# Optimization experiments

Measured on AMD Instinct MI355X. Metric: run time of the kernel, lower is better.

The kernel has to match this reference:

```python
import math
import jax, jax.numpy as jnp
import numpy as np

NUM_HEADS = 12
HEAD_DIM = 64
HIDDEN = NUM_HEADS * HEAD_DIM  # 768
SEQ = 4096


def setup_inputs() -> dict:
    key = jax.random.key(0)
    ks = jax.random.split(key, 7)
    s = 0.02  # BERT-style init scale for weights
    return {
        "hidden_states": jax.random.normal(ks[0], (1, SEQ, HIDDEN), jnp.float32),
        "Wq": jax.random.normal(ks[1], (HIDDEN, HIDDEN), jnp.float32) * s,
        "bq": jax.random.normal(ks[2], (HIDDEN,), jnp.float32) * s,
        "Wk": jax.random.normal(ks[3], (HIDDEN, HIDDEN), jnp.float32) * s,
        "bk": jax.random.normal(ks[4], (HIDDEN,), jnp.float32) * s,
        "Wv": jax.random.normal(ks[5], (HIDDEN, HIDDEN), jnp.float32) * s,
        "bv": jax.random.normal(ks[6], (HIDDEN,), jnp.float32) * s,
    }


def _split_heads(z):
    # [S, HIDDEN] -> [H, S, dh]
    S = z.shape[0]
    return jnp.transpose(z.reshape(S, NUM_HEADS, HEAD_DIM), (1, 0, 2))


def reference(hidden_states, Wq, bq, Wk, bk, Wv, bv):
    # batch is squeezed in the original module (kernel is unbatched)
    x = hidden_states[0]  # [S, D]
    q = _split_heads(x @ Wq.T + bq)  # [H, S, dh]
    k = _split_heads(x @ Wk.T + bk)  # [H, S, dh]
    scale = 1.0 / math.sqrt(HEAD_DIM)
    scores = jnp.einsum('hqd,hkd->hqk', q, k) * scale  # [H, S, S]
    probs = jax.nn.softmax(scores, axis=-1)
    # multi_rand_attn_cuda approximates P @ (x @ Wv^T + bv) via CDF-driven
    # Monte-Carlo column sampling of Wv; its expectation is the exact product,
    # which is the correctness baseline computed here.
    v = _split_heads(x @ Wv.T + bv)  # [H, S, dh]
    ctx = jnp.einsum('hqk,hkd->hqd', probs, v)  # [H, S, dh]
    ctx = jnp.transpose(ctx, (1, 0, 2)).reshape(x.shape[0], HIDDEN)
    return ctx[None]  # [1, S, D]
```

## Files before the change

### kernel.cpp

```cpp
#include <hip/hip_runtime.h>
#include <stdint.h>


typedef float    f32x4 __attribute__((ext_vector_type(4)));
typedef _Float16 h16x8 __attribute__((ext_vector_type(8)));
typedef unsigned short u16;

#define MFMA_F16(A, B, C) __builtin_amdgcn_mfma_f32_16x16x32_f16((A), (B), (C), 0, 0, 0)
#define ZERO4 ((f32x4){0.f, 0.f, 0.f, 0.f})

#define SEQ 4096
#define HID 768
#define NH  12
#define DH  64

__device__ __forceinline__ u16 f2h(float f) {
  union { _Float16 h; u16 u; } v;
  v.h = (_Float16)f;
  return v.u;
}
__device__ __forceinline__ float h2f(u16 u) {
  union { u16 u; _Float16 h; } v;
  v.u = u;
  return (float)v.h;
}

__device__ __forceinline__ void gload_lds16(const void* g, void* l) {
  __builtin_amdgcn_global_load_lds(
      (__attribute__((address_space(1))) void*)(g),
      (__attribute__((address_space(3))) void*)(l),
      16, 0, 0);
}

__global__ __launch_bounds__(256) void cast_all_k(
    const float* __restrict__ x,  const float* __restrict__ wq,
    const float* __restrict__ wk, const float* __restrict__ wv,
    u16* __restrict__ xh,  u16* __restrict__ wqh,
    u16* __restrict__ wkh, u16* __restrict__ wvh)
{
  int i = blockIdx.x * 256 + threadIdx.x;
  const int NX4 = (SEQ * HID) / 4;
  const int NW4 = (HID * HID) / 4;
  const float4* src; ushort4* dst; int idx;
  if (i < NX4) {
    src = (const float4*)x; dst = (ushort4*)xh; idx = i;
  } else {
    int j = i - NX4;
    int w = j / NW4;
    idx = j - w * NW4;
    src = (const float4*)(w == 0 ? wq : (w == 1 ? wk : wv));
    dst = (ushort4*)(w == 0 ? wqh : (w == 1 ? wkh : wvh));
  }
  float4 v = src[idx];
  ushort4 o;
  o.x = f2h(v.x); o.y = f2h(v.y); o.z = f2h(v.z); o.w = f2h(v.w);
  dst[idx] = o;
}

__global__ __launch_bounds__(256, 2) void qkv_gemm_k(
    const u16* __restrict__ xh,
    const u16* __restrict__ wqh, const u16* __restrict__ wkh, const u16* __restrict__ wvh,
    const float* __restrict__ bq, const float* __restrict__ bk, const float* __restrict__ bv,
    u16* __restrict__ Qh, u16* __restrict__ Kh, u16* __restrict__ Vt)
{
  __shared__ u16 As[128 * 32];
  __shared__ u16 Bs[128 * 32];

  const int t = threadIdx.x;
  const int wave = t >> 6, lane = t & 63;
  const int m = lane & 15, quad = lane >> 4;
  const int z  = blockIdx.z;
  const int n0 = blockIdx.x * 128;
  const int m0 = blockIdx.y * 128;

  const u16*   W    = (z == 0) ? wqh : (z == 1) ? wkh : wvh;
  const float* bias = (z == 0) ? bq  : (z == 1) ? bk  : bv;

  const int wm = (wave >> 1) * 64;
  const int wn = (wave & 1) * 64;

  f32x4 acc[4][4];
#pragma unroll
  for (int i = 0; i < 4; i++)
#pragma unroll
    for (int j = 0; j < 4; j++) acc[i][j] = ZERO4;

  const int srow = t >> 2;
  const int sch  = t & 3;
  const u16* gA = xh + (m0 + srow) * HID + sch * 8;
  const u16* gB = W  + (n0 + srow) * HID + sch * 8;
  u16* lA = As + wave * 512;
  u16* lB = Bs + wave * 512;

  for (int k0 = 0; k0 < HID; k0 += 32) {
    __syncthreads();
#pragma unroll
    for (int c = 0; c < 2; c++) {
      gload_lds16(gA + c * 64 * HID + k0, lA + c * 2048);
      gload_lds16(gB + c * 64 * HID + k0, lB + c * 2048);
    }
    __syncthreads();

    h16x8 af[4], bf[4];
#pragma unroll
    for (int i = 0; i < 4; i++)
      af[i] = *(const h16x8*)(As + (wm + i * 16 + m) * 32 + quad * 8);
#pragma unroll
    for (int j = 0; j < 4; j++)
      bf[j] = *(const h16x8*)(Bs + (wn + j * 16 + m) * 32 + quad * 8);
#pragma unroll
    for (int i = 0; i < 4; i++)
#pragma unroll
      for (int j = 0; j < 4; j++)
        acc[i][j] = MFMA_F16(af[i], bf[j], acc[i][j]);
  }

  if (z < 2) {
    u16* outp = (z == 0) ? Qh : Kh;
#pragma unroll
    for (int i = 0; i < 4; i++) {
      int row = m0 + wm + i * 16 + quad * 4;
#pragma unroll
      for (int j = 0; j < 4; j++) {
        int col = n0 + wn + j * 16 + m;
        float bb = bias[col];
#pragma unroll
        for (int r = 0; r < 4; r++)
          outp[(row + r) * HID + col] = f2h(acc[i][j][r] + bb);
      }
    }
  } else {
#pragma unroll
    for (int i = 0; i < 4; i++) {
      int row = m0 + wm + i * 16 + quad * 4;
#pragma unroll
      for (int j = 0; j < 4; j++) {
        int col = n0 + wn + j * 16 + m;
        float bb = bias[col];
        ushort4 o;
        o.x = f2h(acc[i][j][0] + bb);
        o.y = f2h(acc[i][j][1] + bb);
        o.z = f2h(acc[i][j][2] + bb);
        o.w = f2h(acc[i][j][3] + bb);
        *(ushort4*)(Vt + col * SEQ + row) = o;
      }
    }
  }
}

__global__ __launch_bounds__(256, 3) void attn_k(
    const u16* __restrict__ Qh, const u16* __restrict__ Kh, const u16* __restrict__ Vt,
    float* __restrict__ out0, u16* __restrict__ Op1, float* __restrict__ Lp)
{
  __shared__ u16 Ks[128 * 64];
  __shared__ u16 Vs[64 * 128];
  __shared__ u16 Ps[4 * 2048];

  const int t = threadIdx.x;
  const int wave = t >> 6, lane = t & 63;
  const int m = lane & 15, quad = lane >> 4;
  const int h  = blockIdx.y;
  const int q0 = blockIdx.x * 128;
  const int sp = blockIdx.z;
  const int kvbase = sp * 2048;

  h16x8 qf[2][2];
#pragma unroll
  for (int qn = 0; qn < 2; qn++)
#pragma unroll
    for (int ks = 0; ks < 2; ks++)
      qf[qn][ks] = *(const h16x8*)(Qh + (q0 + wave * 32 + qn * 16 + m) * HID
                                   + h * DH + ks * 32 + quad * 8);

  f32x4 O[2][4];
#pragma unroll
  for (int qn = 0; qn < 2; qn++)
#pragma unroll
    for (int jd = 0; jd < 4; jd++) O[qn][jd] = ZERO4;
  float lsum[2] = {0.f, 0.f};

  const int krow_b = wave * 8 + (lane >> 3);
  const int kcl    = lane & 7;
  const int vrow_b = wave * 4 + (lane >> 4);
  const int vcl    = lane & 15;
  u16* Pw = Ps + wave * 2048;

  const float cexp = 0.18033688011112042f;

  for (int it = 0; it < 16; ++it) {
    const int kv0 = kvbase + it * 128;
    __syncthreads();
#pragma unroll
    for (int c = 0; c < 4; c++) {
      int row = c * 32 + krow_b;
      int cg  = kcl ^ (row & 7);
      gload_lds16(Kh + (kv0 + row) * HID + h * DH + cg * 8,
                  Ks + c * 2048 + wave * 512);
      int d  = c * 16 + vrow_b;
      int vg = vcl ^ (d & 15);
      gload_lds16(Vt + (h * DH + d) * SEQ + kv0 + vg * 8,
                  Vs + c * 2048 + wave * 512);
    }
    __syncthreads();

#pragma unroll
    for (int half = 0; half < 2; ++half) {
#pragma unroll
      for (int j4 = 0; j4 < 4; ++j4) {
        const int jt = half * 4 + j4;
        const int krow = jt * 16 + m;
        h16x8 kb0 = *(const h16x8*)(Ks + krow * 64 + ((quad    ) ^ (m & 7)) * 8);
        h16x8 kb1 = *(const h16x8*)(Ks + krow * 64 + ((4 + quad) ^ (m & 7)) * 8);
        f32x4 s0 = MFMA_F16(kb0, qf[0][0], ZERO4);
        s0       = MFMA_F16(kb1, qf[0][1], s0);
        f32x4 s1 = MFMA_F16(kb0, qf[1][0], ZERO4);
        s1       = MFMA_F16(kb1, qf[1][1], s1);

        ushort4 o0, o1;
        {
          float p0 = __builtin_amdgcn_exp2f(s0[0] * cexp);
          float p1 = __builtin_amdgcn_exp2f(s0[1] * cexp);
          float p2 = __builtin_amdgcn_exp2f(s0[2] * cexp);
          float p3 = __builtin_amdgcn_exp2f(s0[3] * cexp);
          lsum[0] += (p0 + p1) + (p2 + p3);
          o0.x = f2h(p0); o0.y = f2h(p1); o0.z = f2h(p2); o0.w = f2h(p3);
        }
        {
          float p0 = __builtin_amdgcn_exp2f(s1[0] * cexp);
          float p1 = __builtin_amdgcn_exp2f(s1[1] * cexp);
          float p2 = __builtin_amdgcn_exp2f(s1[2] * cexp);
          float p3 = __builtin_amdgcn_exp2f(s1[3] * cexp);
          lsum[1] += (p0 + p1) + (p2 + p3);
          o1.x = f2h(p0); o1.y = f2h(p1); o1.z = f2h(p2); o1.w = f2h(p3);
        }
        const int cw = j4 * 2 + (quad >> 1);
        const int sub = (quad & 1) * 4;
        *(ushort4*)(Pw + m * 128 + ((cw    ) ^ m) * 8 + sub) = o0;
        *(ushort4*)(Pw + m * 128 + ((cw + 8) ^ m) * 8 + sub) = o1;
      }

#pragma unroll
      for (int s2 = 0; s2 < 2; ++s2) {
        const int si = half * 2 + s2;
        h16x8 pa0 = *(const h16x8*)(Pw + m * 128 + ((s2 * 4 + quad    ) ^ m) * 8);
        h16x8 pa1 = *(const h16x8*)(Pw + m * 128 + ((s2 * 4 + quad + 8) ^ m) * 8);
#pragma unroll
        for (int jd = 0; jd < 4; ++jd) {
          const int drow = jd * 16 + m;
          h16x8 vb = *(const h16x8*)(Vs + drow * 128 + ((si * 4 + quad) ^ m) * 8);
          O[0][jd] = MFMA_F16(pa0, vb, O[0][jd]);
          O[1][jd] = MFMA_F16(pa1, vb, O[1][jd]);
        }
      }
    }
  }

#pragma unroll
  for (int qn = 0; qn < 2; qn++) {
    float v = lsum[qn];
    v += __shfl_xor(v, 16, 64);
    v += __shfl_xor(v, 32, 64);
    if (quad == 0)
      Lp[sp * NH * SEQ + h * SEQ + q0 + wave * 32 + qn * 16 + m] = v;
#pragma unroll
    for (int jd = 0; jd < 4; jd++) {
      int col = h * DH + jd * 16 + m;
#pragma unroll
      for (int r = 0; r < 4; r++) {
        int row = q0 + wave * 32 + qn * 16 + quad * 4 + r;
        if (sp == 0) out0[row * HID + col] = O[qn][jd][r];
        else         Op1[row * HID + col] = f2h(O[qn][jd][r]);
      }
    }
  }
}

__global__ __launch_bounds__(256) void reduce_k(
    float* __restrict__ out, const u16* __restrict__ Op1,
    const float* __restrict__ Lp)
{
  int i = blockIdx.x * 256 + threadIdx.x;
  int s  = i / 192;
  int c4 = i - s * 192;
  int h  = c4 >> 4;
  float L = Lp[h * SEQ + s] + Lp[NH * SEQ + h * SEQ + s];
  float inv = __builtin_amdgcn_rcpf(L);
  float4 a = ((const float4*)out)[i];
  ushort4 b = ((const ushort4*)Op1)[i];
  float4 r;
  r.x = (a.x + h2f(b.x)) * inv;
  r.y = (a.y + h2f(b.y)) * inv;
  r.z = (a.z + h2f(b.z)) * inv;
  r.w = (a.w + h2f(b.w)) * inv;
  ((float4*)out)[i] = r;
}

extern "C" void kernel_launch(void* const* d_in, const int* in_sizes, int n_in,
                              void* d_out, int out_size, void* d_ws, size_t ws_size,
                              hipStream_t stream) {
  const float* x  = (const float*)d_in[0];
  const float* Wq = (const float*)d_in[1];
  const float* bq = (const float*)d_in[2];
  const float* Wk = (const float*)d_in[3];
  const float* bk = (const float*)d_in[4];
  const float* Wv = (const float*)d_in[5];
  const float* bv = (const float*)d_in[6];
  float* out = (float*)d_out;

  char* ws = (char*)d_ws;
  u16* Qh  = (u16*)(ws);
  u16* Kh  = (u16*)(ws + 6291456);
  u16* Vt  = (u16*)(ws + 12582912);
  u16* xh  = (u16*)(ws + 18874368);
  u16* wqh = (u16*)(ws + 25165824);
  u16* wkh = (u16*)(ws + 26345472);
  u16* wvh = (u16*)(ws + 27525120);
  u16*   Op1 = (u16*)(ws + 18874368);
  float* Lp  = (float*)(ws + 25165824);

  cast_all_k<<<4800, 256, 0, stream>>>(x, Wq, Wk, Wv, xh, wqh, wkh, wvh);
  qkv_gemm_k<<<dim3(6, 32, 3), 256, 0, stream>>>(xh, wqh, wkh, wvh,
                                                 bq, bk, bv, Qh, Kh, Vt);
  attn_k<<<dim3(32, NH, 2), 256, 0, stream>>>(Qh, Kh, Vt, out, Op1, Lp);
  reduce_k<<<3072, 256, 0, stream>>>(out, Op1, Lp);
}
```

Baseline: 178.1 us.

## Keep softmax probabilities in registers and feed them directly to PV MFMA

The attention kernel no longer writes P to shared memory and reads it back. It uses the 16x16x16 MFMA, whose A-operand layout matches the S accumulator layout, so exp'd scores feed the PV product straight from registers. V is stored with a swizzle so the matching B fragments can be read from LDS. The softmax scale is folded into Q at projection time. The block shrinks to 2 waves of 64 query rows each, which raises register pressure and halves the threads loading each KV tile, and the packed conversion uses round-toward-zero.

```diff
diff --git a/kernel.cpp b/kernel.cpp
--- a/kernel.cpp
+++ b/kernel.cpp
@@ -4,15 +4,21 @@
 
 typedef float    f32x4 __attribute__((ext_vector_type(4)));
 typedef _Float16 h16x8 __attribute__((ext_vector_type(8)));
+typedef _Float16 h16x4 __attribute__((ext_vector_type(4)));
+typedef _Float16 h16x2 __attribute__((ext_vector_type(2)));
+typedef __fp16   fp16x2 __attribute__((ext_vector_type(2)));
 typedef unsigned short u16;
 
-#define MFMA_F16(A, B, C) __builtin_amdgcn_mfma_f32_16x16x32_f16((A), (B), (C), 0, 0, 0)
+#define MFMA32(A, B, C) __builtin_amdgcn_mfma_f32_16x16x32_f16((A), (B), (C), 0, 0, 0)
+#define MFMA16(A, B, C) __builtin_amdgcn_mfma_f32_16x16x16f16((A), (B), (C), 0, 0, 0)
 #define ZERO4 ((f32x4){0.f, 0.f, 0.f, 0.f})
 
 #define SEQ 4096
 #define HID 768
 #define NH  12
 #define DH  64
+
+#define CEXP 0.18033688011112042f
 
 __device__ __forceinline__ u16 f2h(float f) {
   union { _Float16 h; u16 u; } v;
@@ -112,11 +118,12 @@
     for (int i = 0; i < 4; i++)
 #pragma unroll
       for (int j = 0; j < 4; j++)
-        acc[i][j] = MFMA_F16(af[i], bf[j], acc[i][j]);
+        acc[i][j] = MFMA32(af[i], bf[j], acc[i][j]);
   }
 
   if (z < 2) {
     u16* outp = (z == 0) ? Qh : Kh;
+    const float sc = (z == 0) ? CEXP : 1.0f;
 #pragma unroll
     for (int i = 0; i < 4; i++) {
       int row = m0 + wm + i * 16 + quad * 4;
@@ -126,7 +133,7 @@
         float bb = bias[col];
 #pragma unroll
         for (int r = 0; r < 4; r++)
-          outp[(row + r) * HID + col] = f2h(acc[i][j][r] + bb);
+          outp[(row + r) * HID + col] = f2h((acc[i][j][r] + bb) * sc);
       }
     }
   } else {
@@ -142,19 +149,19 @@
         o.y = f2h(acc[i][j][1] + bb);
         o.z = f2h(acc[i][j][2] + bb);
         o.w = f2h(acc[i][j][3] + bb);
-        *(ushort4*)(Vt + col * SEQ + row) = o;
-      }
-    }
-  }
-}
-
-__global__ __launch_bounds__(256, 3) void attn_k(
+        int vrow = row ^ ((col & 8) ? 4 : 0);
+        *(ushort4*)(Vt + col * SEQ + vrow) = o;
+      }
+    }
+  }
+}
+
+__global__ __launch_bounds__(128, 2) void attn_k(
     const u16* __restrict__ Qh, const u16* __restrict__ Kh, const u16* __restrict__ Vt,
     float* __restrict__ out0, u16* __restrict__ Op1, float* __restrict__ Lp)
 {
   __shared__ u16 Ks[128 * 64];
   __shared__ u16 Vs[64 * 128];
-  __shared__ u16 Ps[4 * 2048];
 
   const int t = threadIdx.x;
   const int wave = t >> 6, lane = t & 63;
@@ -164,110 +171,96 @@
   const int sp = blockIdx.z;
   const int kvbase = sp * 2048;
 
-  h16x8 qf[2][2];
-#pragma unroll
-  for (int qn = 0; qn < 2; qn++)
+  h16x8 qf[4][2];
+#pragma unroll
+  for (int qn = 0; qn < 4; qn++)
 #pragma unroll
     for (int ks = 0; ks < 2; ks++)
-      qf[qn][ks] = *(const h16x8*)(Qh + (q0 + wave * 32 + qn * 16 + m) * HID
+      qf[qn][ks] = *(const h16x8*)(Qh + (q0 + wave * 64 + qn * 16 + m) * HID
                                    + h * DH + ks * 32 + quad * 8);
 
-  f32x4 O[2][4];
-#pragma unroll
-  for (int qn = 0; qn < 2; qn++)
+  f32x4 O[4][4];
+#pragma unroll
+  for (int qn = 0; qn < 4; qn++)
 #pragma unroll
     for (int jd = 0; jd < 4; jd++) O[qn][jd] = ZERO4;
-  float lsum[2] = {0.f, 0.f};
+  float lsum[4] = {0.f, 0.f, 0.f, 0.f};
 
   const int krow_b = wave * 8 + (lane >> 3);
   const int kcl    = lane & 7;
   const int vrow_b = wave * 4 + (lane >> 4);
   const int vcl    = lane & 15;
-  u16* Pw = Ps + wave * 2048;
-
-  const float cexp = 0.18033688011112042f;
+  const int vsub   = ((quad & 1) ^ ((m >> 3) & 1)) * 4;
 
   for (int it = 0; it < 16; ++it) {
     const int kv0 = kvbase + it * 128;
     __syncthreads();
 #pragma unroll
-    for (int c = 0; c < 4; c++) {
-      int row = c * 32 + krow_b;
+    for (int c = 0; c < 8; c++) {
+      int row = c * 16 + krow_b;
       int cg  = kcl ^ (row & 7);
       gload_lds16(Kh + (kv0 + row) * HID + h * DH + cg * 8,
-                  Ks + c * 2048 + wave * 512);
-      int d  = c * 16 + vrow_b;
+                  Ks + c * 1024 + wave * 512);
+      int d  = c * 8 + vrow_b;
       int vg = vcl ^ (d & 15);
       gload_lds16(Vt + (h * DH + d) * SEQ + kv0 + vg * 8,
-                  Vs + c * 2048 + wave * 512);
+                  Vs + c * 1024 + wave * 512);
     }
     __syncthreads();
 
 #pragma unroll
-    for (int half = 0; half < 2; ++half) {
-#pragma unroll
-      for (int j4 = 0; j4 < 4; ++j4) {
-        const int jt = half * 4 + j4;
-        const int krow = jt * 16 + m;
-        h16x8 kb0 = *(const h16x8*)(Ks + krow * 64 + ((quad    ) ^ (m & 7)) * 8);
-        h16x8 kb1 = *(const h16x8*)(Ks + krow * 64 + ((4 + quad) ^ (m & 7)) * 8);
-        f32x4 s0 = MFMA_F16(kb0, qf[0][0], ZERO4);
-        s0       = MFMA_F16(kb1, qf[0][1], s0);
-        f32x4 s1 = MFMA_F16(kb0, qf[1][0], ZERO4);
-        s1       = MFMA_F16(kb1, qf[1][1], s1);
-
-        ushort4 o0, o1;
-        {
-          float p0 = __builtin_amdgcn_exp2f(s0[0] * cexp);
-          float p1 = __builtin_amdgcn_exp2f(s0[1] * cexp);
-          float p2 = __builtin_amdgcn_exp2f(s0[2] * cexp);
-          float p3 = __builtin_amdgcn_exp2f(s0[3] * cexp);
-          lsum[0] += (p0 + p1) + (p2 + p3);
-          o0.x = f2h(p0); o0.y = f2h(p1); o0.z = f2h(p2); o0.w = f2h(p3);
-        }
-        {
-          float p0 = __builtin_amdgcn_exp2f(s1[0] * cexp);
-          float p1 = __builtin_amdgcn_exp2f(s1[1] * cexp);
-          float p2 = __builtin_amdgcn_exp2f(s1[2] * cexp);
-          float p3 = __builtin_amdgcn_exp2f(s1[3] * cexp);
-          lsum[1] += (p0 + p1) + (p2 + p3);
-          o1.x = f2h(p0); o1.y = f2h(p1); o1.z = f2h(p2); o1.w = f2h(p3);
-        }
-        const int cw = j4 * 2 + (quad >> 1);
-        const int sub = (quad & 1) * 4;
-        *(ushort4*)(Pw + m * 128 + ((cw    ) ^ m) * 8 + sub) = o0;
-        *(ushort4*)(Pw + m * 128 + ((cw + 8) ^ m) * 8 + sub) = o1;
-      }
-
-#pragma unroll
-      for (int s2 = 0; s2 < 2; ++s2) {
-        const int si = half * 2 + s2;
-        h16x8 pa0 = *(const h16x8*)(Pw + m * 128 + ((s2 * 4 + quad    ) ^ m) * 8);
-        h16x8 pa1 = *(const h16x8*)(Pw + m * 128 + ((s2 * 4 + quad + 8) ^ m) * 8);
-#pragma unroll
-        for (int jd = 0; jd < 4; ++jd) {
-          const int drow = jd * 16 + m;
-          h16x8 vb = *(const h16x8*)(Vs + drow * 128 + ((si * 4 + quad) ^ m) * 8);
-          O[0][jd] = MFMA_F16(pa0, vb, O[0][jd]);
-          O[1][jd] = MFMA_F16(pa1, vb, O[1][jd]);
-        }
-      }
-    }
-  }
-
-#pragma unroll
-  for (int qn = 0; qn < 2; qn++) {
+    for (int j = 0; j < 8; ++j) {
+      const int krow = j * 16 + m;
+      h16x8 kb0 = *(const h16x8*)(Ks + krow * 64 + ((quad    ) ^ (m & 7)) * 8);
+      h16x8 kb1 = *(const h16x8*)(Ks + krow * 64 + ((4 + quad) ^ (m & 7)) * 8);
+
+      f32x4 S[4];
+#pragma unroll
+      for (int qn = 0; qn < 4; qn++) {
+        S[qn] = MFMA32(kb0, qf[qn][0], ZERO4);
+        S[qn] = MFMA32(kb1, qf[qn][1], S[qn]);
+      }
+
+      h16x4 vb[4];
+#pragma unroll
+      for (int jd = 0; jd < 4; jd++) {
+        int d = jd * 16 + m;
+        vb[jd] = *(const h16x4*)(Vs + d * 128
+                                 + (((j * 2 + (quad >> 1)) ^ m) * 8) + vsub);
+      }
+
+#pragma unroll
+      for (int qn = 0; qn < 4; qn++) {
+        float e0 = __builtin_amdgcn_exp2f(S[qn][0]);
+        float e1 = __builtin_amdgcn_exp2f(S[qn][1]);
+        float e2 = __builtin_amdgcn_exp2f(S[qn][2]);
+        float e3 = __builtin_amdgcn_exp2f(S[qn][3]);
+        lsum[qn] += (e0 + e1) + (e2 + e3);
+        fp16x2 p01 = __builtin_amdgcn_cvt_pkrtz(e0, e1);
+        fp16x2 p23 = __builtin_amdgcn_cvt_pkrtz(e2, e3);
+        h16x2 q01 = __builtin_bit_cast(h16x2, p01);
+        h16x2 q23 = __builtin_bit_cast(h16x2, p23);
+        h16x4 pa  = __builtin_shufflevector(q01, q23, 0, 1, 2, 3);
+#pragma unroll
+        for (int jd = 0; jd < 4; jd++)
+          O[qn][jd] = MFMA16(pa, vb[jd], O[qn][jd]);
+      }
+    }
+  }
+
+#pragma unroll
+  for (int qn = 0; qn < 4; qn++) {
     float v = lsum[qn];
     v += __shfl_xor(v, 16, 64);
     v += __shfl_xor(v, 32, 64);
     if (quad == 0)
-      Lp[sp * NH * SEQ + h * SEQ + q0 + wave * 32 + qn * 16 + m] = v;
+      Lp[sp * NH * SEQ + h * SEQ + q0 + wave * 64 + qn * 16 + m] = v;
 #pragma unroll
     for (int jd = 0; jd < 4; jd++) {
       int col = h * DH + jd * 16 + m;
 #pragma unroll
       for (int r = 0; r < 4; r++) {
-        int row = q0 + wave * 32 + qn * 16 + quad * 4 + r;
+        int row = q0 + wave * 64 + qn * 16 + quad * 4 + r;
         if (sp == 0) out0[row * HID + col] = O[qn][jd][r];
         else         Op1[row * HID + col] = f2h(O[qn][jd][r]);
       }
@@ -321,6 +314,6 @@
   cast_all_k<<<4800, 256, 0, stream>>>(x, Wq, Wk, Wv, xh, wqh, wkh, wvh);
   qkv_gemm_k<<<dim3(6, 32, 3), 256, 0, stream>>>(xh, wqh, wkh, wvh,
                                                  bq, bk, bv, Qh, Kh, Vt);
-  attn_k<<<dim3(32, NH, 2), 256, 0, stream>>>(Qh, Kh, Vt, out, Op1, Lp);
+  attn_k<<<dim3(32, NH, 2), 128, 0, stream>>>(Qh, Kh, Vt, out, Op1, Lp);
   reduce_k<<<3072, 256, 0, stream>>>(out, Op1, Lp);
 }
```

New measurement: 205.6 us. 1.15x slower.
